# Kernel optimization log

Hardware: AMD Instinct MI355X
Metric: run time of the kernel (lower is better)

Reference implementation:

```python
import jax, jax.numpy as jnp
import numpy as np

B, D, H = 32768, 688, 4
DH = D // H          # 172 head dim (d_model // h, overrides ctor d_k)
MH = 128             # mlp hidden
EPS = 1e-5
SCALE = 1.0 / float(np.sqrt(DH))


def _ln(x, g, b):
    m = jnp.mean(x, -1, keepdims=True)
    v = jnp.var(x, -1, keepdims=True)  # biased var, matches torch LayerNorm
    return (x - m) / jnp.sqrt(v + EPS) * g + b


def setup_inputs() -> dict:
    key = jax.random.key(0)
    ks = jax.random.split(key, 16)
    w = lambda k, o, i: jax.random.normal(k, (o, i), jnp.float32) * 0.001  # init.normal_(std=0.001)
    z = lambda n: jnp.zeros((n,), jnp.float32)
    o = lambda n: jnp.ones((n,), jnp.float32)
    return dict(
        x=jax.random.normal(ks[0], (B, D), jnp.float32),
        x2=jax.random.normal(ks[1], (B, D), jnp.float32),
        Wq_v=w(ks[2], D, D), bq_v=z(D),
        Wk_v=w(ks[3], D, D), bk_v=z(D),
        Wv_v=w(ks[4], D, D), bv_v=z(D),
        Wq_i=w(ks[5], D, D), bq_i=z(D),
        Wk_i=w(ks[6], D, D), bk_i=z(D),
        Wv_i=w(ks[7], D, D), bv_i=z(D),
        Wo_v=w(ks[8], D, D), bo_v=z(D),
        Wo_i=w(ks[9], D, D), bo_i=z(D),
        ln1_g=o(D), ln1_b=z(D), ln2_g=o(D), ln2_b=z(D),
        ln3_g=o(D), ln3_b=z(D), ln4_g=o(D), ln4_b=z(D),
        m1v_W=w(ks[10], MH, D), m1v_b=z(MH),
        m2v_W=w(ks[11], D, MH), m2v_b=z(D),
        m1i_W=w(ks[12], MH, D), m1i_b=z(MH),
        m2i_W=w(ks[13], D, MH), m2i_b=z(D),
        coef=o(8),  # LearnableCoefficient 1..8, all init to 1.0
    )


def reference(x, x2,
              Wq_v, bq_v, Wk_v, bk_v, Wv_v, bv_v,
              Wq_i, bq_i, Wk_i, bk_i, Wv_i, bv_i,
              Wo_v, bo_v, Wo_i, bo_i,
              ln1_g, ln1_b, ln2_g, ln2_b, ln3_g, ln3_b, ln4_g, ln4_b,
              m1v_W, m1v_b, m2v_W, m2v_b, m1i_W, m1i_b, m2i_W, m2i_b,
              coef):
    rgb = _ln(x, ln1_g, ln1_b)
    ir = _ln(x2, ln2_g, ln2_b)
    proj = lambda t, W, b: (t @ W.T + b).reshape(-1, H, DH)  # (B, h, d_k)
    q_vis, k_vis, v_vis = proj(rgb, Wq_v, bq_v), proj(rgb, Wk_v, bk_v), proj(rgb, Wv_v, bv_v)
    q_ir, k_ir, v_ir = proj(ir, Wq_i, bq_i), proj(ir, Wk_i, bk_i), proj(ir, Wv_i, bv_i)
    # cross attention over heads: scores are (B, h, h)
    att_vis = jax.nn.softmax(jnp.einsum('bhd,bgd->bhg', q_ir, k_vis) * SCALE, -1)
    att_ir = jax.nn.softmax(jnp.einsum('bhd,bgd->bhg', q_vis, k_ir) * SCALE, -1)
    out_vis = jnp.einsum('bhg,bgd->bhd', att_vis, v_vis).reshape(-1, D) @ Wo_v.T + bo_v
    out_ir = jnp.einsum('bhg,bgd->bhd', att_ir, v_ir).reshape(-1, D) @ Wo_i.T + bo_i
    out_vis = coef[0] * x + coef[1] * out_vis
    out_ir = coef[2] * x2 + coef[3] * out_ir
    mv = jax.nn.gelu(_ln(out_vis, ln3_g, ln3_b) @ m1v_W.T + m1v_b, approximate=False) @ m2v_W.T + m2v_b
    mi = jax.nn.gelu(_ln(out_ir, ln4_g, ln4_b) @ m1i_W.T + m1i_b, approximate=False) @ m2i_W.T + m2i_b
    out_vis = coef[4] * out_vis + coef[5] * mv
    out_ir = coef[6] * out_ir + coef[7] * mi
    return out_vis, out_ir
```

## Files before the change

kernel.cpp:

```cpp
#include <hip/hip_runtime.h>
#include <cmath>


#define B_ROWS 32768
#define D_DIM  688
#define DP     704
#define DH_DIM 172
#define MH_DIM 128

typedef unsigned short ushort_t;
typedef __attribute__((ext_vector_type(8))) __bf16 bf16x8;
typedef __attribute__((ext_vector_type(4))) float  f32x4;

__device__ __forceinline__ float b2f(ushort_t u) {
    return __builtin_bit_cast(float, (unsigned int)u << 16);
}
__device__ __forceinline__ ushort_t f2bf(float f) {
    unsigned int u = __builtin_bit_cast(unsigned int, f);
    u += 0x7FFFu + ((u >> 16) & 1u);
    return (ushort_t)(u >> 16);
}

__device__ __forceinline__ void gl2lds16(const ushort_t* g, ushort_t* l) {
    __builtin_amdgcn_global_load_lds(
        (const __attribute__((address_space(1))) unsigned int*)g,
        (__attribute__((address_space(3))) unsigned int*)l, 16, 0, 0);
}

struct CvtJobs {
    const float* src[12];
    ushort_t*    dst[12];
    int O[12], Opad[12], Kin[12], Kpad[12];
    int bstart[13];
};

__global__ __launch_bounds__(256)
void cvt_all(CvtJobs jobs)
{
    int b = blockIdx.x;
    int j = 0;
    while (b >= jobs.bstart[j + 1]) ++j;
    const int t = (b - jobs.bstart[j]) * 256 + threadIdx.x;
    const int Kpad = jobs.Kpad[j];
    const int Kin  = jobs.Kin[j];
    const int cpr  = Kpad >> 3;
    if (t >= jobs.Opad[j] * cpr) return;
    const int o = t / cpr;
    const int c = t - o * cpr;
    unsigned int p0 = 0, p1 = 0, p2 = 0, p3 = 0;
    if (o < jobs.O[j] && (c * 8 + 8) <= Kin) {
        const float* s = jobs.src[j] + (size_t)o * Kin + c * 8;
        float4 f0 = reinterpret_cast<const float4*>(s)[0];
        float4 f1 = reinterpret_cast<const float4*>(s)[1];
        p0 = f2bf(f0.x) | ((unsigned int)f2bf(f0.y) << 16);
        p1 = f2bf(f0.z) | ((unsigned int)f2bf(f0.w) << 16);
        p2 = f2bf(f1.x) | ((unsigned int)f2bf(f1.y) << 16);
        p3 = f2bf(f1.z) | ((unsigned int)f2bf(f1.w) << 16);
    }
    *reinterpret_cast<uint4*>(jobs.dst[j] + (size_t)o * Kpad + c * 8) =
        make_uint4(p0, p1, p2, p3);
}

__global__ __launch_bounds__(256)
void pack_bias(const float* __restrict__ a0, const float* __restrict__ a1,
               const float* __restrict__ a2, const float* __restrict__ b0,
               const float* __restrict__ b1, const float* __restrict__ b2,
               float* __restrict__ dv, float* __restrict__ di)
{
    int t = blockIdx.x * 256 + threadIdx.x;
    if (t >= 2064) return;
    float v, w;
    if (t < 688)       { v = a0[t];        w = b0[t]; }
    else if (t < 1376) { v = a1[t - 688];  w = b1[t - 688]; }
    else               { v = a2[t - 1376]; w = b2[t - 1376]; }
    dv[t] = v; di[t] = w;
}

__global__ __launch_bounds__(256)
void ln_kernel(const float* __restrict__ Xv, const float* __restrict__ Xi,
               const float* __restrict__ gv, const float* __restrict__ bv,
               const float* __restrict__ gi, const float* __restrict__ bi,
               ushort_t* __restrict__ Yv, ushort_t* __restrict__ Yi)
{
    const int lane = threadIdx.x & 63;
    const int wave = threadIdx.x >> 6;
    const long w = (long)blockIdx.x * 4 + wave;
    const float* X; const float* g; const float* b; ushort_t* Y; long r;
    if (w < B_ROWS) { X = Xv; g = gv; b = bv; Y = Yv; r = w; }
    else            { X = Xi; g = gi; b = bi; Y = Yi; r = w - B_ROWS; }

    const float4* row = reinterpret_cast<const float4*>(X + r * D_DIM);
    float4 v0 = row[lane];
    float4 v1 = row[lane + 64];
    float4 v2 = make_float4(0.f, 0.f, 0.f, 0.f);
    if (lane < 44) v2 = row[lane + 128];

    float s  = v0.x + v0.y + v0.z + v0.w + v1.x + v1.y + v1.z + v1.w
             + v2.x + v2.y + v2.z + v2.w;
    float s2 = v0.x*v0.x + v0.y*v0.y + v0.z*v0.z + v0.w*v0.w
             + v1.x*v1.x + v1.y*v1.y + v1.z*v1.z + v1.w*v1.w
             + v2.x*v2.x + v2.y*v2.y + v2.z*v2.z + v2.w*v2.w;
#pragma unroll
    for (int m = 32; m; m >>= 1) { s += __shfl_xor(s, m); s2 += __shfl_xor(s2, m); }

    const float mean = s * (1.f / 688.f);
    const float var  = s2 * (1.f / 688.f) - mean * mean;
    const float rstd = rsqrtf(var + 1e-5f);

    const float4* g4 = reinterpret_cast<const float4*>(g);
    const float4* b4 = reinterpret_cast<const float4*>(b);
    ushort4* out4 = reinterpret_cast<ushort4*>(Y + r * DP);

    {
        float4 gg = g4[lane], bb = b4[lane];
        ushort4 o;
        o.x = f2bf((v0.x - mean) * rstd * gg.x + bb.x);
        o.y = f2bf((v0.y - mean) * rstd * gg.y + bb.y);
        o.z = f2bf((v0.z - mean) * rstd * gg.z + bb.z);
        o.w = f2bf((v0.w - mean) * rstd * gg.w + bb.w);
        out4[lane] = o;
    }
    {
        float4 gg = g4[lane + 64], bb = b4[lane + 64];
        ushort4 o;
        o.x = f2bf((v1.x - mean) * rstd * gg.x + bb.x);
        o.y = f2bf((v1.y - mean) * rstd * gg.y + bb.y);
        o.z = f2bf((v1.z - mean) * rstd * gg.z + bb.z);
        o.w = f2bf((v1.w - mean) * rstd * gg.w + bb.w);
        out4[lane + 64] = o;
    }
    if (lane < 44) {
        float4 gg = g4[lane + 128], bb = b4[lane + 128];
        ushort4 o;
        o.x = f2bf((v2.x - mean) * rstd * gg.x + bb.x);
        o.y = f2bf((v2.y - mean) * rstd * gg.y + bb.y);
        o.z = f2bf((v2.z - mean) * rstd * gg.z + bb.z);
        o.w = f2bf((v2.w - mean) * rstd * gg.w + bb.w);
        out4[lane + 128] = o;
    } else if (lane < 48) {
        out4[lane + 128] = make_ushort4(0, 0, 0, 0);
    }
}

template<int MODE>
__global__ __launch_bounds__(512, 2)
void gemmT(const ushort_t* __restrict__ A0, const ushort_t* __restrict__ A1,
           const ushort_t* __restrict__ W0, const ushort_t* __restrict__ W1,
           const float* __restrict__ bias0, const float* __restrict__ bias1,
           ushort_t* __restrict__ out0, ushort_t* __restrict__ out1,
           const float* __restrict__ res0, const float* __restrict__ res1,
           const float* __restrict__ coef, int ca0, int cb0, int ca1, int cb1,
           int NBn, int N, int K, int lda, int ldw, int ldo)
{
    __shared__ __align__(16) ushort_t lds[36864];

    const int q8 = gridDim.x >> 3;
    const int v  = (blockIdx.x & 7) * q8 + (blockIdx.x >> 3);
    const int nb = v % NBn;
    const int tmp = v / NBn;
    const int mb = tmp & 127;
    const int zz = tmp >> 7;

    const ushort_t* A = zz ? A1 : A0;
    const ushort_t* W = zz ? W1 : W0;
    const float* bias = zz ? bias1 : bias0;
    ushort_t* outp    = zz ? out1 : out0;
    const float* resid = zz ? res1 : res0;
    const int ca = zz ? ca1 : ca0;
    const int cb = zz ? cb1 : cb0;

    const int tid  = threadIdx.x;
    const int lane = tid & 63;
    const int wave = tid >> 6;
    const int wrow = wave >> 1;
    const int wcol = wave & 1;
    const int m0 = mb * 256;
    const int n0 = nb * 128;
    const int rl16 = lane & 15;
    const int q4   = lane >> 4;

    const int r0a  = tid >> 2;
    const int swzk = ((tid & 3) ^ ((tid >> 3) & 3)) * 8;

    f32x4 acc[4][4];
#pragma unroll
    for (int i = 0; i < 4; ++i)
#pragma unroll
        for (int j = 0; j < 4; ++j)
            acc[i][j] = f32x4{0.f, 0.f, 0.f, 0.f};

    const int NT = K >> 5;

#define STAGET(kt, bb) do {                                                        \
    const ushort_t* _sa = A + (size_t)(m0 + r0a) * lda + (kt)*32 + swzk;           \
    gl2lds16(_sa,                    lds + (bb)*12288 + wave*512);                 \
    gl2lds16(_sa + 128*(size_t)lda,  lds + (bb)*12288 + 4096 + wave*512);          \
    const ushort_t* _sb = W + (size_t)(n0 + r0a) * ldw + (kt)*32 + swzk;           \
    gl2lds16(_sb,                    lds + (bb)*12288 + 8192 + wave*512);          \
} while (0)

    STAGET(0, 0);
    STAGET(1, 1);
    asm volatile("s_waitcnt vmcnt(3)" ::: "memory");
    __builtin_amdgcn_s_barrier();

    for (int t = 0; t < NT; ++t) {
        const int cbuf = t % 3;
        const int pbuf = (t + 2) % 3;
        const int tn2 = (t + 2 < NT) ? t + 2 : NT - 1;

        bf16x8 af[4], bw[4];
#pragma unroll
        for (int i = 0; i < 4; ++i) {
            const int row_ = wrow * 64 + i * 16 + rl16;
            af[i] = *reinterpret_cast<const bf16x8*>(
                lds + cbuf * 12288 + row_ * 32 + ((q4 ^ ((row_ >> 1) & 3)) * 8));
        }
#pragma unroll
        for (int j = 0; j < 4; ++j) {
            const int row_ = wcol * 64 + j * 16 + rl16;
            bw[j] = *reinterpret_cast<const bf16x8*>(
                lds + cbuf * 12288 + 8192 + row_ * 32 + ((q4 ^ ((row_ >> 1) & 3)) * 8));
        }
        STAGET(tn2, pbuf);
        asm volatile("s_waitcnt vmcnt(3)" ::: "memory");
        __builtin_amdgcn_s_barrier();
        __builtin_amdgcn_s_setprio(1);
#pragma unroll
        for (int i = 0; i < 4; ++i)
#pragma unroll
            for (int j = 0; j < 4; ++j)
                acc[i][j] = __builtin_amdgcn_mfma_f32_16x16x32_bf16(af[i], bw[j], acc[i][j], 0, 0, 0);
        __builtin_amdgcn_s_setprio(0);
        __builtin_amdgcn_s_barrier();
    }

    asm volatile("s_waitcnt vmcnt(0)" ::: "memory");
    __builtin_amdgcn_s_barrier();

    ushort_t* const Cl = lds;
#pragma unroll
    for (int mi = 0; mi < 4; ++mi)
#pragma unroll
        for (int nj = 0; nj < 4; ++nj)
#pragma unroll
            for (int r = 0; r < 4; ++r) {
                const int row  = wrow * 64 + mi * 16 + q4 * 4 + r;
                const int colL = wcol * 64 + nj * 16 + rl16;
                const int blk  = (colL >> 3) ^ (((row >> 2) & 3) << 1);
                Cl[row * 128 + blk * 8 + (colL & 7)] = f2bf(acc[mi][nj][r]);
            }
    __syncthreads();

    float cA = 0.f, cB = 1.f;
    if constexpr (MODE == 1) { cA = coef[ca]; cB = coef[cb]; }
#pragma unroll
    for (int it2 = 0; it2 < 8; ++it2) {
        const int c   = it2 * 512 + tid;
        const int row = c >> 4;
        const int lb  = c & 15;
        const int gcol = n0 + lb * 8;
        if (gcol >= N) continue;
        const int pb = lb ^ (((row >> 2) & 3) << 1);
        uint4 pv = *reinterpret_cast<const uint4*>(Cl + row * 128 + pb * 8);
        const ushort_t* pu = (const ushort_t*)&pv;
        float4 b0 = *reinterpret_cast<const float4*>(bias + gcol);
        float4 b1 = *reinterpret_cast<const float4*>(bias + gcol + 4);
        const float bb[8] = {b0.x, b0.y, b0.z, b0.w, b1.x, b1.y, b1.z, b1.w};
        const size_t idx = (size_t)(m0 + row) * ldo + gcol;
        ushort_t o[8];
        if constexpr (MODE == 0) {
#pragma unroll
            for (int k = 0; k < 8; ++k) o[k] = f2bf(b2f(pu[k]) + bb[k]);
        } else {
            const float* rp = resid + idx;
            float4 r0_ = reinterpret_cast<const float4*>(rp)[0];
            float4 r1_ = reinterpret_cast<const float4*>(rp)[1];
            const float rr[8] = {r0_.x, r0_.y, r0_.z, r0_.w, r1_.x, r1_.y, r1_.z, r1_.w};
#pragma unroll
            for (int k = 0; k < 8; ++k)
                o[k] = f2bf(cA * rr[k] + cB * (b2f(pu[k]) + bb[k]));
        }
        *reinterpret_cast<uint4*>(outp + idx) = *reinterpret_cast<uint4*>(o);
    }
#undef STAGET
}

__global__ __launch_bounds__(256)
void mlp_fused(const ushort_t* __restrict__ ov0, const ushort_t* __restrict__ ov1,
               const float* __restrict__ g0, const float* __restrict__ b0,
               const float* __restrict__ g1, const float* __restrict__ b1,
               const ushort_t* __restrict__ W10, const ushort_t* __restrict__ W11,
               const float* __restrict__ mb10, const float* __restrict__ mb11,
               const ushort_t* __restrict__ W20, const ushort_t* __restrict__ W21,
               const float* __restrict__ mb20, const float* __restrict__ mb21,
               const float* __restrict__ coef,
               float* __restrict__ out0, float* __restrict__ out1)
{
    __shared__ __align__(16) ushort_t hraw[32 * 712];
    __shared__ __align__(16) ushort_t gbuf[32 * 136];
    __shared__ float glds[704];
    __shared__ float blds[704];
    __shared__ float mlds[32];
    __shared__ float rlds[32];

    const int zz = blockIdx.y;
    const ushort_t* ovb = zz ? ov1 : ov0;
    const float* lg = zz ? g1 : g0;
    const float* lb = zz ? b1 : b0;
    const ushort_t* W1 = zz ? W11 : W10;
    const float* mb1 = zz ? mb11 : mb10;
    const ushort_t* W2 = zz ? W21 : W20;
    const float* mb2 = zz ? mb21 : mb20;
    float* outp = zz ? out1 : out0;
    const float cA = coef[zz ? 6 : 4];
    const float cB = coef[zz ? 7 : 5];

    const int tid  = threadIdx.x;
    const int lane = tid & 63;
    const int wv   = tid >> 6;
    const long r0  = (long)blockIdx.x * 32;

    if (tid < 176) {
        float4 gg = make_float4(0, 0, 0, 0), bb = make_float4(0, 0, 0, 0);
        if (tid < 172) {
            gg = reinterpret_cast<const float4*>(lg)[tid];
            bb = reinterpret_cast<const float4*>(lb)[tid];
        }
        reinterpret_cast<float4*>(glds)[tid] = gg;
        reinterpret_cast<float4*>(blds)[tid] = bb;
    }

#pragma unroll
    for (int it = 0; it < 11; ++it) {
        const int c = it * 256 + tid;
        const int row = c / 88;
        const int u = c - row * 88;
        uint4 vv = make_uint4(0, 0, 0, 0);
        if (u < 86)
            vv = *reinterpret_cast<const uint4*>(ovb + (r0 + row) * 688 + u * 8);
        *reinterpret_cast<uint4*>(&hraw[row * 712 + u * 8]) = vv;
    }
    __syncthreads();

    for (int rr = 0; rr < 8; ++rr) {
        const int row = wv * 8 + rr;
        const ushort_t* hp = &hraw[row * 712];
        ushort4 a0 = *reinterpret_cast<const ushort4*>(hp + lane * 4);
        ushort4 a1 = *reinterpret_cast<const ushort4*>(hp + 256 + lane * 4);
        ushort4 a2 = make_ushort4(0, 0, 0, 0);
        if (lane < 44) a2 = *reinterpret_cast<const ushort4*>(hp + 512 + lane * 4);
        float e[12] = {b2f(a0.x), b2f(a0.y), b2f(a0.z), b2f(a0.w),
                       b2f(a1.x), b2f(a1.y), b2f(a1.z), b2f(a1.w),
                       b2f(a2.x), b2f(a2.y), b2f(a2.z), b2f(a2.w)};
        float s = 0.f, s2 = 0.f;
#pragma unroll
        for (int k = 0; k < 12; ++k) { s += e[k]; s2 += e[k] * e[k]; }
#pragma unroll
        for (int m = 32; m; m >>= 1) { s += __shfl_xor(s, m); s2 += __shfl_xor(s2, m); }
        if (lane == 0) {
            const float mean = s * (1.f / 688.f);
            const float var  = s2 * (1.f / 688.f) - mean * mean;
            mlds[row] = mean;
            rlds[row] = rsqrtf(var + 1e-5f);
        }
    }
    __syncthreads();

#pragma unroll
    for (int it = 0; it < 11; ++it) {
        const int c = it * 256 + tid;
        if (c < 2752) {
            const int row = c / 86;
            const int u = c - row * 86;
            uint4 vv = *reinterpret_cast<const uint4*>(&hraw[row * 712 + u * 8]);
            const float mean = mlds[row], rstd = rlds[row];
            const ushort_t* pe = (const ushort_t*)&vv;
            ushort_t o[8];
#pragma unroll
            for (int k = 0; k < 8; ++k)
                o[k] = f2bf((b2f(pe[k]) - mean) * rstd * glds[u * 8 + k] + blds[u * 8 + k]);
            *reinterpret_cast<uint4*>(&hraw[row * 712 + u * 8]) = *reinterpret_cast<uint4*>(o);
        }
    }
    __syncthreads();

    const int rl16 = lane & 15;
    const int q4   = lane >> 4;

    {
        f32x4 acc[2][2];
#pragma unroll
        for (int i = 0; i < 2; ++i) { acc[i][0] = f32x4{0,0,0,0}; acc[i][1] = f32x4{0,0,0,0}; }
        for (int kt = 0; kt < 11; ++kt) {
#pragma unroll
            for (int kk = 0; kk < 64; kk += 32) {
                bf16x8 af[2], bw[2];
#pragma unroll
                for (int n = 0; n < 2; ++n)
                    bw[n] = *reinterpret_cast<const bf16x8*>(
                        W1 + (size_t)(wv * 32 + n * 16 + rl16) * 704 + kt * 64 + kk + q4 * 8);
#pragma unroll
                for (int i = 0; i < 2; ++i)
                    af[i] = *reinterpret_cast<const bf16x8*>(
                        &hraw[(i * 16 + rl16) * 712 + kt * 64 + kk + q4 * 8]);
#pragma unroll
                for (int i = 0; i < 2; ++i)
#pragma unroll
                    for (int n = 0; n < 2; ++n)
                        acc[i][n] = __builtin_amdgcn_mfma_f32_16x16x32_bf16(
                            af[i], bw[n], acc[i][n], 0, 0, 0);
            }
        }
        const int rb = q4 * 4;
#pragma unroll
        for (int n = 0; n < 2; ++n) {
            const int col = wv * 32 + n * 16 + rl16;
            const float bc = mb1[col];
#pragma unroll
            for (int i = 0; i < 2; ++i)
#pragma unroll
                for (int r = 0; r < 4; ++r) {
                    float val = acc[i][n][r] + bc;
                    val = 0.5f * val * (1.0f + erff(val * 0.70710678118654752f));
                    gbuf[(i * 16 + rb + r) * 136 + col] = f2bf(val);
                }
        }
    }
    __syncthreads();

    for (int ch = 0; ch < 11; ++ch) {
        const int col16 = wv * 176 + ch * 16;
        if (col16 >= 688) continue;
        f32x4 acc2[2];
        acc2[0] = f32x4{0, 0, 0, 0};
        acc2[1] = f32x4{0, 0, 0, 0};
#pragma unroll
        for (int kk = 0; kk < 4; ++kk) {
            bf16x8 bw2 = *reinterpret_cast<const bf16x8*>(
                W2 + (size_t)(col16 + rl16) * 128 + kk * 32 + q4 * 8);
            bf16x8 af2[2];
#pragma unroll
            for (int i = 0; i < 2; ++i)
                af2[i] = *reinterpret_cast<const bf16x8*>(
                    &gbuf[(i * 16 + rl16) * 136 + kk * 32 + q4 * 8]);
#pragma unroll
            for (int i = 0; i < 2; ++i)
                acc2[i] = __builtin_amdgcn_mfma_f32_16x16x32_bf16(af2[i], bw2, acc2[i], 0, 0, 0);
        }
        const int col = col16 + rl16;
        const float bc = mb2[col];
#pragma unroll
        for (int i = 0; i < 2; ++i)
#pragma unroll
            for (int r = 0; r < 4; ++r) {
                const long row = r0 + i * 16 + q4 * 4 + r;
                const float raw = b2f(ovb[row * 688 + col]);
                outp[row * 688 + col] = cA * raw + cB * (acc2[i][r] + bc);
            }
    }
}

__global__ __launch_bounds__(256)
void attn_kernel(const ushort_t* __restrict__ qkv_v, const ushort_t* __restrict__ qkv_i,
                 ushort_t* __restrict__ ctx_v, ushort_t* __restrict__ ctx_i)
{
    const int lane = threadIdx.x & 63;
    const int wave = threadIdx.x >> 6;
    const long r = (long)blockIdx.x * 4 + wave;
    const ushort_t* bv = qkv_v + r * 2064;
    const ushort_t* bi = qkv_i + r * 2064;

    float sv[4][4], si[4][4];
#pragma unroll
    for (int h = 0; h < 4; ++h)
#pragma unroll
        for (int g = 0; g < 4; ++g) { sv[h][g] = 0.f; si[h][g] = 0.f; }

    float vvr[3][4], vir[3][4];
#pragma unroll
    for (int it = 0; it < 3; ++it) {
        const int d = lane + it * 64;
        const bool ok = d < DH_DIM;
        float qv[4], kv[4], qi[4], ki[4];
#pragma unroll
        for (int h = 0; h < 4; ++h) {
            const int o = h * DH_DIM + d;
            qv[h]      = ok ? b2f(bv[o]) : 0.f;
            kv[h]      = ok ? b2f(bv[D_DIM + o]) : 0.f;
            vvr[it][h] = ok ? b2f(bv[2 * D_DIM + o]) : 0.f;
            qi[h]      = ok ? b2f(bi[o]) : 0.f;
            ki[h]      = ok ? b2f(bi[D_DIM + o]) : 0.f;
            vir[it][h] = ok ? b2f(bi[2 * D_DIM + o]) : 0.f;
        }
#pragma unroll
        for (int h = 0; h < 4; ++h)
#pragma unroll
            for (int g = 0; g < 4; ++g) {
                sv[h][g] += qi[h] * kv[g];
                si[h][g] += qv[h] * ki[g];
            }
    }

#pragma unroll
    for (int h = 0; h < 4; ++h)
#pragma unroll
        for (int g = 0; g < 4; ++g) {
            float a = sv[h][g], b = si[h][g];
#pragma unroll
            for (int m = 32; m; m >>= 1) { a += __shfl_xor(a, m); b += __shfl_xor(b, m); }
            sv[h][g] = a; si[h][g] = b;
        }

    const float scale = 0.07624928516630235f;
    float av[4][4], ai[4][4];
#pragma unroll
    for (int h = 0; h < 4; ++h) {
        float m1 = fmaxf(fmaxf(sv[h][0], sv[h][1]), fmaxf(sv[h][2], sv[h][3])) * scale;
        float m2 = fmaxf(fmaxf(si[h][0], si[h][1]), fmaxf(si[h][2], si[h][3])) * scale;
        float d1 = 0.f, d2 = 0.f;
#pragma unroll
        for (int g = 0; g < 4; ++g) {
            av[h][g] = expf(sv[h][g] * scale - m1); d1 += av[h][g];
            ai[h][g] = expf(si[h][g] * scale - m2); d2 += ai[h][g];
        }
        const float r1 = 1.f / d1, r2 = 1.f / d2;
#pragma unroll
        for (int g = 0; g < 4; ++g) { av[h][g] *= r1; ai[h][g] *= r2; }
    }

#pragma unroll
    for (int it = 0; it < 3; ++it) {
        const int d = lane + it * 64;
        if (d < DH_DIM) {
#pragma unroll
            for (int h = 0; h < 4; ++h) {
                float cv = av[h][0] * vvr[it][0] + av[h][1] * vvr[it][1]
                         + av[h][2] * vvr[it][2] + av[h][3] * vvr[it][3];
                float ci = ai[h][0] * vir[it][0] + ai[h][1] * vir[it][1]
                         + ai[h][2] * vir[it][2] + ai[h][3] * vir[it][3];
                ctx_v[r * DP + h * DH_DIM + d] = f2bf(cv);
                ctx_i[r * DP + h * DH_DIM + d] = f2bf(ci);
            }
        }
    }
    if (lane < 16) {
        ctx_v[r * DP + 688 + lane] = 0;
        ctx_i[r * DP + 688 + lane] = 0;
    }
}

extern "C" void kernel_launch(void* const* d_in, const int* in_sizes, int n_in,
                              void* d_out, int out_size, void* d_ws, size_t ws_size,
                              hipStream_t stream)
{
    if (n_in < 35) return;
    const float* x     = (const float*)d_in[0];
    const float* x2    = (const float*)d_in[1];
    const float* Wq_v  = (const float*)d_in[2];
    const float* bq_v  = (const float*)d_in[3];
    const float* Wk_v  = (const float*)d_in[4];
    const float* bk_v  = (const float*)d_in[5];
    const float* Wv_v  = (const float*)d_in[6];
    const float* bv_v  = (const float*)d_in[7];
    const float* Wq_i  = (const float*)d_in[8];
    const float* bq_i  = (const float*)d_in[9];
    const float* Wk_i  = (const float*)d_in[10];
    const float* bk_i  = (const float*)d_in[11];
    const float* Wv_i  = (const float*)d_in[12];
    const float* bv_i  = (const float*)d_in[13];
    const float* Wo_v  = (const float*)d_in[14];
    const float* bo_v  = (const float*)d_in[15];
    const float* Wo_i  = (const float*)d_in[16];
    const float* bo_i  = (const float*)d_in[17];
    const float* ln1_g = (const float*)d_in[18];
    const float* ln1_b = (const float*)d_in[19];
    const float* ln2_g = (const float*)d_in[20];
    const float* ln2_b = (const float*)d_in[21];
    const float* ln3_g = (const float*)d_in[22];
    const float* ln3_b = (const float*)d_in[23];
    const float* ln4_g = (const float*)d_in[24];
    const float* ln4_b = (const float*)d_in[25];
    const float* m1v_W = (const float*)d_in[26];
    const float* m1v_b = (const float*)d_in[27];
    const float* m2v_W = (const float*)d_in[28];
    const float* m2v_b = (const float*)d_in[29];
    const float* m1i_W = (const float*)d_in[30];
    const float* m1i_b = (const float*)d_in[31];
    const float* m2i_W = (const float*)d_in[32];
    const float* m2i_b = (const float*)d_in[33];
    const float* coef  = (const float*)d_in[34];

    const size_t BDP = (size_t)B_ROWS * DP;
    const size_t BD  = (size_t)B_ROWS * D_DIM;

    char* ws = (char*)d_ws;
    size_t off = 0;
    auto give = [&](size_t bytes) {
        char* p = ws + off;
        off += (bytes + 255) & ~(size_t)255;
        return p;
    };
    ushort_t* Wcat_v = (ushort_t*)give(2304ull * DP * 2);
    ushort_t* Wcat_i = (ushort_t*)give(2304ull * DP * 2);
    ushort_t* Wo_vb  = (ushort_t*)give(768ull * DP * 2);
    ushort_t* Wo_ib  = (ushort_t*)give(768ull * DP * 2);
    ushort_t* m1vb   = (ushort_t*)give(128ull * DP * 2);
    ushort_t* m1ib   = (ushort_t*)give(128ull * DP * 2);
    ushort_t* m2vb   = (ushort_t*)give(768ull * 128 * 2);
    ushort_t* m2ib   = (ushort_t*)give(768ull * 128 * 2);
    float*    bcat_v = (float*)give(2064 * 4);
    float*    bcat_i = (float*)give(2064 * 4);
    char* regX = give(BDP * 2 * 2);
    char* regQ = give((size_t)B_ROWS * 2064 * 2 * 2);
    if (ws_size < off) return;

    ushort_t* xn_v  = (ushort_t*)regX;
    ushort_t* xn_i  = xn_v + BDP;
    ushort_t* ctx_v = xn_v;
    ushort_t* ctx_i = xn_i;
    ushort_t* qkv_v = (ushort_t*)regQ;
    ushort_t* qkv_i = qkv_v + (size_t)B_ROWS * 2064;
    ushort_t* ovb   = (ushort_t*)regQ;
    ushort_t* oib   = ovb + BD;

    float* ov = (float*)d_out;
    float* oi = ov + BD;

    CvtJobs J;
    const float* srcs[12] = {Wq_v, Wk_v, Wv_v, Wq_i, Wk_i, Wv_i,
                             Wo_v, Wo_i, m1v_W, m1i_W, m2v_W, m2i_W};
    ushort_t* dsts[12] = {Wcat_v, Wcat_v + 688 * DP, Wcat_v + 1376 * DP,
                          Wcat_i, Wcat_i + 688 * DP, Wcat_i + 1376 * DP,
                          Wo_vb, Wo_ib, m1vb, m1ib, m2vb, m2ib};
    int Os[12]    = {688, 688, 688, 688, 688, 688, 688, 688, 128, 128, 688, 688};
    int Opads[12] = {688, 688, 800, 688, 688, 800, 768, 768, 128, 128, 768, 768};
    int Kins[12]  = {688, 688, 688, 688, 688, 688, 688, 688, 688, 688, 128, 128};
    int Kpads[12] = {DP, DP, DP, DP, DP, DP, DP, DP, DP, DP, 128, 128};
    int bs = 0;
    for (int j = 0; j < 12; ++j) {
        J.src[j] = srcs[j]; J.dst[j] = dsts[j];
        J.O[j] = Os[j]; J.Opad[j] = Opads[j]; J.Kin[j] = Kins[j]; J.Kpad[j] = Kpads[j];
        J.bstart[j] = bs;
        bs += (Opads[j] * (Kpads[j] >> 3) + 255) / 256;
    }
    J.bstart[12] = bs;
    cvt_all<<<dim3(bs), dim3(256), 0, stream>>>(J);

    pack_bias<<<dim3(9), dim3(256), 0, stream>>>(bq_v, bk_v, bv_v, bq_i, bk_i, bv_i,
                                                 bcat_v, bcat_i);

    ln_kernel<<<dim3(2 * B_ROWS / 4), dim3(256), 0, stream>>>(
        x, x2, ln1_g, ln1_b, ln2_g, ln2_b, xn_v, xn_i);

    gemmT<0><<<dim3(128 * 17 * 2), dim3(512), 0, stream>>>(
        xn_v, xn_i, Wcat_v, Wcat_i, bcat_v, bcat_i, qkv_v, qkv_i,
        nullptr, nullptr, nullptr, 0, 0, 0, 0, 17, 2064, DP, DP, DP, 2064);

    attn_kernel<<<dim3(B_ROWS / 4), dim3(256), 0, stream>>>(qkv_v, qkv_i, ctx_v, ctx_i);

    gemmT<1><<<dim3(128 * 6 * 2), dim3(512), 0, stream>>>(
        ctx_v, ctx_i, Wo_vb, Wo_ib, bo_v, bo_i, ovb, oib,
        x, x2, coef, 0, 1, 2, 3, 6, 688, DP, DP, DP, 688);

    mlp_fused<<<dim3(B_ROWS / 32, 2), dim3(256), 0, stream>>>(
        ovb, oib, ln3_g, ln3_b, ln4_g, ln4_b,
        m1vb, m1ib, m1v_b, m1i_b, m2vb, m2ib, m2v_b, m2i_b,
        coef, ov, oi);
}
```

Measured before the change: 689.7 us.

## Halve GEMM block to 4 waves with larger per-wave tiles; stage attention rows via LDS

The GEMM now runs 256 threads per block for the same 256x128 tile. Each wave computes a 128x64 sub-tile with 8x4 MFMA accumulators and issues twice as many async global-to-LDS loads per stage, with the wait counts adjusted to match. This aims for more MFMA work per LDS fragment load and fewer waves contending for barriers, at the cost of higher register pressure. Separately, the attention kernel bulk-copies its four rows of qkv into LDS and has each lane read 4-wide vectors of 4 consecutive head-dim elements, replacing scalar strided global loads and stores with vectorized ones.

Result: slower. 717.4 us (+4.0%).

```diff
diff --git a/kernel.cpp b/kernel.cpp
--- a/kernel.cpp
+++ b/kernel.cpp
@@ -143,7 +143,7 @@
 }
 
 template<int MODE>
-__global__ __launch_bounds__(512, 2)
+__global__ __launch_bounds__(256, 2)
 void gemmT(const ushort_t* __restrict__ A0, const ushort_t* __restrict__ A1,
            const ushort_t* __restrict__ W0, const ushort_t* __restrict__ W1,
            const float* __restrict__ bias0, const float* __restrict__ bias1,
@@ -179,12 +179,12 @@
     const int rl16 = lane & 15;
     const int q4   = lane >> 4;
 
-    const int r0a  = tid >> 2;
-    const int swzk = ((tid & 3) ^ ((tid >> 3) & 3)) * 8;
-
-    f32x4 acc[4][4];
-#pragma unroll
-    for (int i = 0; i < 4; ++i)
+    const int r0a  = (wave * 64 + lane) >> 2;
+    const int swzk = ((lane & 3) ^ ((lane >> 3) & 3)) * 8;
+
+    f32x4 acc[8][4];
+#pragma unroll
+    for (int i = 0; i < 8; ++i)
 #pragma unroll
         for (int j = 0; j < 4; ++j)
             acc[i][j] = f32x4{0.f, 0.f, 0.f, 0.f};
@@ -192,16 +192,19 @@
     const int NT = K >> 5;
 
 #define STAGET(kt, bb) do {                                                        \
-    const ushort_t* _sa = A + (size_t)(m0 + r0a) * lda + (kt)*32 + swzk;           \
-    gl2lds16(_sa,                    lds + (bb)*12288 + wave*512);                 \
-    gl2lds16(_sa + 128*(size_t)lda,  lds + (bb)*12288 + 4096 + wave*512);          \
-    const ushort_t* _sb = W + (size_t)(n0 + r0a) * ldw + (kt)*32 + swzk;           \
-    gl2lds16(_sb,                    lds + (bb)*12288 + 8192 + wave*512);          \
+    const ushort_t* _a = A + (size_t)(m0 + r0a) * lda + (kt)*32 + swzk;            \
+    gl2lds16(_a,                     lds + (bb)*12288 + wave*512);                 \
+    gl2lds16(_a +  64*(size_t)lda,   lds + (bb)*12288 + 2048 + wave*512);          \
+    gl2lds16(_a + 128*(size_t)lda,   lds + (bb)*12288 + 4096 + wave*512);          \
+    gl2lds16(_a + 192*(size_t)lda,   lds + (bb)*12288 + 6144 + wave*512);          \
+    const ushort_t* _b = W + (size_t)(n0 + r0a) * ldw + (kt)*32 + swzk;            \
+    gl2lds16(_b,                     lds + (bb)*12288 + 8192 + wave*512);          \
+    gl2lds16(_b +  64*(size_t)ldw,   lds + (bb)*12288 + 10240 + wave*512);         \
 } while (0)
 
     STAGET(0, 0);
     STAGET(1, 1);
-    asm volatile("s_waitcnt vmcnt(3)" ::: "memory");
+    asm volatile("s_waitcnt vmcnt(6)" ::: "memory");
     __builtin_amdgcn_s_barrier();
 
     for (int t = 0; t < NT; ++t) {
@@ -209,10 +212,10 @@
         const int pbuf = (t + 2) % 3;
         const int tn2 = (t + 2 < NT) ? t + 2 : NT - 1;
 
-        bf16x8 af[4], bw[4];
-#pragma unroll
-        for (int i = 0; i < 4; ++i) {
-            const int row_ = wrow * 64 + i * 16 + rl16;
+        bf16x8 af[8], bw[4];
+#pragma unroll
+        for (int i = 0; i < 8; ++i) {
+            const int row_ = wrow * 128 + i * 16 + rl16;
             af[i] = *reinterpret_cast<const bf16x8*>(
                 lds + cbuf * 12288 + row_ * 32 + ((q4 ^ ((row_ >> 1) & 3)) * 8));
         }
@@ -223,11 +226,11 @@
                 lds + cbuf * 12288 + 8192 + row_ * 32 + ((q4 ^ ((row_ >> 1) & 3)) * 8));
         }
         STAGET(tn2, pbuf);
-        asm volatile("s_waitcnt vmcnt(3)" ::: "memory");
+        asm volatile("s_waitcnt vmcnt(6)" ::: "memory");
         __builtin_amdgcn_s_barrier();
         __builtin_amdgcn_s_setprio(1);
 #pragma unroll
-        for (int i = 0; i < 4; ++i)
+        for (int i = 0; i < 8; ++i)
 #pragma unroll
             for (int j = 0; j < 4; ++j)
                 acc[i][j] = __builtin_amdgcn_mfma_f32_16x16x32_bf16(af[i], bw[j], acc[i][j], 0, 0, 0);
@@ -240,12 +243,12 @@
 
     ushort_t* const Cl = lds;
 #pragma unroll
-    for (int mi = 0; mi < 4; ++mi)
+    for (int mi = 0; mi < 8; ++mi)
 #pragma unroll
         for (int nj = 0; nj < 4; ++nj)
 #pragma unroll
             for (int r = 0; r < 4; ++r) {
-                const int row  = wrow * 64 + mi * 16 + q4 * 4 + r;
+                const int row  = wrow * 128 + mi * 16 + q4 * 4 + r;
                 const int colL = wcol * 64 + nj * 16 + rl16;
                 const int blk  = (colL >> 3) ^ (((row >> 2) & 3) << 1);
                 Cl[row * 128 + blk * 8 + (colL & 7)] = f2bf(acc[mi][nj][r]);
@@ -255,8 +258,8 @@
     float cA = 0.f, cB = 1.f;
     if constexpr (MODE == 1) { cA = coef[ca]; cB = coef[cb]; }
 #pragma unroll
-    for (int it2 = 0; it2 < 8; ++it2) {
-        const int c   = it2 * 512 + tid;
+    for (int it2 = 0; it2 < 16; ++it2) {
+        const int c   = it2 * 256 + tid;
         const int row = c >> 4;
         const int lb  = c & 15;
         const int gcol = n0 + lb * 8;
@@ -465,48 +468,61 @@
 void attn_kernel(const ushort_t* __restrict__ qkv_v, const ushort_t* __restrict__ qkv_i,
                  ushort_t* __restrict__ ctx_v, ushort_t* __restrict__ ctx_i)
 {
-    const int lane = threadIdx.x & 63;
-    const int wave = threadIdx.x >> 6;
-    const long r = (long)blockIdx.x * 4 + wave;
-    const ushort_t* bv = qkv_v + r * 2064;
-    const ushort_t* bi = qkv_i + r * 2064;
+    __shared__ __align__(16) ushort_t sm[16896];
+
+    const int tid  = threadIdx.x;
+    const int lane = tid & 63;
+    const int wv   = tid >> 6;
+    const long r0  = (long)blockIdx.x * 4;
+
+#pragma unroll
+    for (int i = 0; i < 9; ++i) {
+        int c = i * 256 + wv * 64 + lane;
+        if (c > 2063) c = 2063;
+        const int row = c / 516;
+        const int s = c - row * 516;
+        const ushort_t* src = (s < 258)
+            ? qkv_v + (r0 + row) * 2064 + s * 8
+            : qkv_i + (r0 + row) * 2064 + (s - 258) * 8;
+        gl2lds16(src, sm + (size_t)(i * 256 + wv * 64) * 8);
+    }
+    __syncthreads();
+
+    const ushort_t* bv = sm + wv * 4128;
+    const ushort_t* bi = bv + 2064;
+    const bool act = lane < 43;
+    const int d4 = lane * 4;
+
+    float qv[4][4], kv[4][4], vv[4][4], qi[4][4], ki[4][4], vi[4][4];
+#pragma unroll
+    for (int h = 0; h < 4; ++h) {
+        const int o = h * DH_DIM + d4;
+        ushort4 z = make_ushort4(0, 0, 0, 0);
+        ushort4 a = act ? *reinterpret_cast<const ushort4*>(bv + o)        : z;
+        ushort4 b = act ? *reinterpret_cast<const ushort4*>(bv + 688 + o)  : z;
+        ushort4 c = act ? *reinterpret_cast<const ushort4*>(bv + 1376 + o) : z;
+        ushort4 d = act ? *reinterpret_cast<const ushort4*>(bi + o)        : z;
+        ushort4 e = act ? *reinterpret_cast<const ushort4*>(bi + 688 + o)  : z;
+        ushort4 f = act ? *reinterpret_cast<const ushort4*>(bi + 1376 + o) : z;
+        qv[h][0]=b2f(a.x); qv[h][1]=b2f(a.y); qv[h][2]=b2f(a.z); qv[h][3]=b2f(a.w);
+        kv[h][0]=b2f(b.x); kv[h][1]=b2f(b.y); kv[h][2]=b2f(b.z); kv[h][3]=b2f(b.w);
+        vv[h][0]=b2f(c.x); vv[h][1]=b2f(c.y); vv[h][2]=b2f(c.z); vv[h][3]=b2f(c.w);
+        qi[h][0]=b2f(d.x); qi[h][1]=b2f(d.y); qi[h][2]=b2f(d.z); qi[h][3]=b2f(d.w);
+        ki[h][0]=b2f(e.x); ki[h][1]=b2f(e.y); ki[h][2]=b2f(e.z); ki[h][3]=b2f(e.w);
+        vi[h][0]=b2f(f.x); vi[h][1]=b2f(f.y); vi[h][2]=b2f(f.z); vi[h][3]=b2f(f.w);
+    }
 
     float sv[4][4], si[4][4];
 #pragma unroll
     for (int h = 0; h < 4; ++h)
 #pragma unroll
-        for (int g = 0; g < 4; ++g) { sv[h][g] = 0.f; si[h][g] = 0.f; }
-
-    float vvr[3][4], vir[3][4];
-#pragma unroll
-    for (int it = 0; it < 3; ++it) {
-        const int d = lane + it * 64;
-        const bool ok = d < DH_DIM;
-        float qv[4], kv[4], qi[4], ki[4];
-#pragma unroll
-        for (int h = 0; h < 4; ++h) {
-            const int o = h * DH_DIM + d;
-            qv[h]      = ok ? b2f(bv[o]) : 0.f;
-            kv[h]      = ok ? b2f(bv[D_DIM + o]) : 0.f;
-            vvr[it][h] = ok ? b2f(bv[2 * D_DIM + o]) : 0.f;
-            qi[h]      = ok ? b2f(bi[o]) : 0.f;
-            ki[h]      = ok ? b2f(bi[D_DIM + o]) : 0.f;
-            vir[it][h] = ok ? b2f(bi[2 * D_DIM + o]) : 0.f;
-        }
-#pragma unroll
-        for (int h = 0; h < 4; ++h)
-#pragma unroll
-            for (int g = 0; g < 4; ++g) {
-                sv[h][g] += qi[h] * kv[g];
-                si[h][g] += qv[h] * ki[g];
+        for (int g = 0; g < 4; ++g) {
+            float a = 0.f, b = 0.f;
+#pragma unroll
+            for (int e = 0; e < 4; ++e) {
+                a += qi[h][e] * kv[g][e];
+                b += qv[h][e] * ki[g][e];
             }
-    }
-
-#pragma unroll
-    for (int h = 0; h < 4; ++h)
-#pragma unroll
-        for (int g = 0; g < 4; ++g) {
-            float a = sv[h][g], b = si[h][g];
 #pragma unroll
             for (int m = 32; m; m >>= 1) { a += __shfl_xor(a, m); b += __shfl_xor(b, m); }
             sv[h][g] = a; si[h][g] = b;
@@ -529,24 +545,27 @@
         for (int g = 0; g < 4; ++g) { av[h][g] *= r1; ai[h][g] *= r2; }
     }
 
-#pragma unroll
-    for (int it = 0; it < 3; ++it) {
-        const int d = lane + it * 64;
-        if (d < DH_DIM) {
-#pragma unroll
-            for (int h = 0; h < 4; ++h) {
-                float cv = av[h][0] * vvr[it][0] + av[h][1] * vvr[it][1]
-                         + av[h][2] * vvr[it][2] + av[h][3] * vvr[it][3];
-                float ci = ai[h][0] * vir[it][0] + ai[h][1] * vir[it][1]
-                         + ai[h][2] * vir[it][2] + ai[h][3] * vir[it][3];
-                ctx_v[r * DP + h * DH_DIM + d] = f2bf(cv);
-                ctx_i[r * DP + h * DH_DIM + d] = f2bf(ci);
+    const long r = r0 + wv;
+#pragma unroll
+    for (int h = 0; h < 4; ++h) {
+        if (act) {
+            ushort4 ov_, oi_;
+            float c0, c1;
+#pragma unroll
+            for (int e = 0; e < 4; ++e) {
+                c0 = av[h][0]*vv[0][e] + av[h][1]*vv[1][e] + av[h][2]*vv[2][e] + av[h][3]*vv[3][e];
+                c1 = ai[h][0]*vi[0][e] + ai[h][1]*vi[1][e] + ai[h][2]*vi[2][e] + ai[h][3]*vi[3][e];
+                ((ushort_t*)&ov_)[e] = f2bf(c0);
+                ((ushort_t*)&oi_)[e] = f2bf(c1);
             }
-        }
-    }
-    if (lane < 16) {
-        ctx_v[r * DP + 688 + lane] = 0;
-        ctx_i[r * DP + 688 + lane] = 0;
+            *reinterpret_cast<ushort4*>(ctx_v + r * DP + h * DH_DIM + d4) = ov_;
+            *reinterpret_cast<ushort4*>(ctx_i + r * DP + h * DH_DIM + d4) = oi_;
+        }
+    }
+    if (lane >= 44 && lane < 48) {
+        const int o = 688 + (lane - 44) * 4;
+        *reinterpret_cast<ushort4*>(ctx_v + r * DP + o) = make_ushort4(0, 0, 0, 0);
+        *reinterpret_cast<ushort4*>(ctx_i + r * DP + o) = make_ushort4(0, 0, 0, 0);
     }
 }
 
@@ -653,13 +672,13 @@
     ln_kernel<<<dim3(2 * B_ROWS / 4), dim3(256), 0, stream>>>(
         x, x2, ln1_g, ln1_b, ln2_g, ln2_b, xn_v, xn_i);
 
-    gemmT<0><<<dim3(128 * 17 * 2), dim3(512), 0, stream>>>(
+    gemmT<0><<<dim3(128 * 17 * 2), dim3(256), 0, stream>>>(
         xn_v, xn_i, Wcat_v, Wcat_i, bcat_v, bcat_i, qkv_v, qkv_i,
         nullptr, nullptr, nullptr, 0, 0, 0, 0, 17, 2064, DP, DP, DP, 2064);
 
     attn_kernel<<<dim3(B_ROWS / 4), dim3(256), 0, stream>>>(qkv_v, qkv_i, ctx_v, ctx_i);
 
-    gemmT<1><<<dim3(128 * 6 * 2), dim3(512), 0, stream>>>(
+    gemmT<1><<<dim3(128 * 6 * 2), dim3(256), 0, stream>>>(
         ctx_v, ctx_i, Wo_vb, Wo_ib, bo_v, bo_i, ovb, oib,
         x, x2, coef, 0, 1, 2, 3, 6, 688, DP, DP, DP, 688);
 
```

## Halve GEMM block to 4 waves with 128x64 warp tiles and prefetched fragments

Applied to the files above, without the earlier changes.

The bf16 GEMM kernel now uses 256 threads (4 waves) per block, and each wave computes a 128x64 output tile (8x4 MFMA accumulators) instead of 64x64. Global-to-LDS staging is spread over six loads per thread. LDS fragment reads for the next k-step are issued after the current MFMAs, which removes the trailing barrier per iteration. The aim is higher MFMA-to-LDS-read reuse and less barrier overhead per step. In exchange, accumulator register pressure doubles, which may cut occupancy or cause spills.

Result: no change. 685.3 us (-0.6%).

```diff
diff --git a/kernel.cpp b/kernel.cpp
--- a/kernel.cpp
+++ b/kernel.cpp
@@ -143,7 +143,7 @@
 }
 
 template<int MODE>
-__global__ __launch_bounds__(512, 2)
+__global__ __launch_bounds__(256, 2)
 void gemmT(const ushort_t* __restrict__ A0, const ushort_t* __restrict__ A1,
            const ushort_t* __restrict__ W0, const ushort_t* __restrict__ W1,
            const float* __restrict__ bias0, const float* __restrict__ bias1,
@@ -179,12 +179,12 @@
     const int rl16 = lane & 15;
     const int q4   = lane >> 4;
 
-    const int r0a  = tid >> 2;
-    const int swzk = ((tid & 3) ^ ((tid >> 3) & 3)) * 8;
-
-    f32x4 acc[4][4];
-#pragma unroll
-    for (int i = 0; i < 4; ++i)
+    const int r0a  = (wave * 64 + lane) >> 2;
+    const int swzk = ((lane & 3) ^ ((lane >> 3) & 3)) * 8;
+
+    f32x4 acc[8][4];
+#pragma unroll
+    for (int i = 0; i < 8; ++i)
 #pragma unroll
         for (int j = 0; j < 4; ++j)
             acc[i][j] = f32x4{0.f, 0.f, 0.f, 0.f};
@@ -192,60 +192,64 @@
     const int NT = K >> 5;
 
 #define STAGET(kt, bb) do {                                                        \
-    const ushort_t* _sa = A + (size_t)(m0 + r0a) * lda + (kt)*32 + swzk;           \
-    gl2lds16(_sa,                    lds + (bb)*12288 + wave*512);                 \
-    gl2lds16(_sa + 128*(size_t)lda,  lds + (bb)*12288 + 4096 + wave*512);          \
-    const ushort_t* _sb = W + (size_t)(n0 + r0a) * ldw + (kt)*32 + swzk;           \
-    gl2lds16(_sb,                    lds + (bb)*12288 + 8192 + wave*512);          \
+    const ushort_t* _a = A + (size_t)(m0 + r0a) * lda + (kt)*32 + swzk;            \
+    gl2lds16(_a,                     lds + (bb)*12288 + wave*512);                 \
+    gl2lds16(_a +  64*(size_t)lda,   lds + (bb)*12288 + 2048 + wave*512);          \
+    gl2lds16(_a + 128*(size_t)lda,   lds + (bb)*12288 + 4096 + wave*512);          \
+    gl2lds16(_a + 192*(size_t)lda,   lds + (bb)*12288 + 6144 + wave*512);          \
+    const ushort_t* _b = W + (size_t)(n0 + r0a) * ldw + (kt)*32 + swzk;            \
+    gl2lds16(_b,                     lds + (bb)*12288 + 8192 + wave*512);          \
+    gl2lds16(_b +  64*(size_t)ldw,   lds + (bb)*12288 + 10240 + wave*512);         \
 } while (0)
+
+#define RDFRAG(bb) do {                                                            \
+    _Pragma("unroll")                                                              \
+    for (int i = 0; i < 8; ++i) {                                                  \
+        const int row_ = wrow * 128 + i * 16 + rl16;                               \
+        af[i] = *reinterpret_cast<const bf16x8*>(                                  \
+            lds + (bb) * 12288 + row_ * 32 + ((q4 ^ ((row_ >> 1) & 3)) * 8));      \
+    }                                                                              \
+    _Pragma("unroll")                                                              \
+    for (int j = 0; j < 4; ++j) {                                                  \
+        const int row_ = wcol * 64 + j * 16 + rl16;                                \
+        bw[j] = *reinterpret_cast<const bf16x8*>(                                  \
+            lds + (bb) * 12288 + 8192 + row_ * 32 + ((q4 ^ ((row_ >> 1) & 3)) * 8)); \
+    } } while (0)
+
+    bf16x8 af[8], bw[4];
 
     STAGET(0, 0);
     STAGET(1, 1);
-    asm volatile("s_waitcnt vmcnt(3)" ::: "memory");
+    asm volatile("s_waitcnt vmcnt(6)" ::: "memory");
     __builtin_amdgcn_s_barrier();
+    RDFRAG(0);
 
     for (int t = 0; t < NT; ++t) {
-        const int cbuf = t % 3;
-        const int pbuf = (t + 2) % 3;
         const int tn2 = (t + 2 < NT) ? t + 2 : NT - 1;
-
-        bf16x8 af[4], bw[4];
-#pragma unroll
-        for (int i = 0; i < 4; ++i) {
-            const int row_ = wrow * 64 + i * 16 + rl16;
-            af[i] = *reinterpret_cast<const bf16x8*>(
-                lds + cbuf * 12288 + row_ * 32 + ((q4 ^ ((row_ >> 1) & 3)) * 8));
-        }
-#pragma unroll
-        for (int j = 0; j < 4; ++j) {
-            const int row_ = wcol * 64 + j * 16 + rl16;
-            bw[j] = *reinterpret_cast<const bf16x8*>(
-                lds + cbuf * 12288 + 8192 + row_ * 32 + ((q4 ^ ((row_ >> 1) & 3)) * 8));
-        }
-        STAGET(tn2, pbuf);
-        asm volatile("s_waitcnt vmcnt(3)" ::: "memory");
+        STAGET(tn2, (t + 2) % 3);
+        asm volatile("s_waitcnt vmcnt(6)" ::: "memory");
+        asm volatile("s_waitcnt lgkmcnt(0)" ::: "memory");
         __builtin_amdgcn_s_barrier();
         __builtin_amdgcn_s_setprio(1);
 #pragma unroll
-        for (int i = 0; i < 4; ++i)
+        for (int i = 0; i < 8; ++i)
 #pragma unroll
             for (int j = 0; j < 4; ++j)
                 acc[i][j] = __builtin_amdgcn_mfma_f32_16x16x32_bf16(af[i], bw[j], acc[i][j], 0, 0, 0);
         __builtin_amdgcn_s_setprio(0);
-        __builtin_amdgcn_s_barrier();
-    }
-
-    asm volatile("s_waitcnt vmcnt(0)" ::: "memory");
-    __builtin_amdgcn_s_barrier();
+        if (t + 1 < NT) RDFRAG((t + 1) % 3);
+    }
+
+    __syncthreads();
 
     ushort_t* const Cl = lds;
 #pragma unroll
-    for (int mi = 0; mi < 4; ++mi)
+    for (int mi = 0; mi < 8; ++mi)
 #pragma unroll
         for (int nj = 0; nj < 4; ++nj)
 #pragma unroll
             for (int r = 0; r < 4; ++r) {
-                const int row  = wrow * 64 + mi * 16 + q4 * 4 + r;
+                const int row  = wrow * 128 + mi * 16 + q4 * 4 + r;
                 const int colL = wcol * 64 + nj * 16 + rl16;
                 const int blk  = (colL >> 3) ^ (((row >> 2) & 3) << 1);
                 Cl[row * 128 + blk * 8 + (colL & 7)] = f2bf(acc[mi][nj][r]);
@@ -255,8 +259,8 @@
     float cA = 0.f, cB = 1.f;
     if constexpr (MODE == 1) { cA = coef[ca]; cB = coef[cb]; }
 #pragma unroll
-    for (int it2 = 0; it2 < 8; ++it2) {
-        const int c   = it2 * 512 + tid;
+    for (int it2 = 0; it2 < 16; ++it2) {
+        const int c   = it2 * 256 + tid;
         const int row = c >> 4;
         const int lb  = c & 15;
         const int gcol = n0 + lb * 8;
@@ -284,6 +288,7 @@
         *reinterpret_cast<uint4*>(outp + idx) = *reinterpret_cast<uint4*>(o);
     }
 #undef STAGET
+#undef RDFRAG
 }
 
 __global__ __launch_bounds__(256)
@@ -653,13 +658,13 @@
     ln_kernel<<<dim3(2 * B_ROWS / 4), dim3(256), 0, stream>>>(
         x, x2, ln1_g, ln1_b, ln2_g, ln2_b, xn_v, xn_i);
 
-    gemmT<0><<<dim3(128 * 17 * 2), dim3(512), 0, stream>>>(
+    gemmT<0><<<dim3(128 * 17 * 2), dim3(256), 0, stream>>>(
         xn_v, xn_i, Wcat_v, Wcat_i, bcat_v, bcat_i, qkv_v, qkv_i,
         nullptr, nullptr, nullptr, 0, 0, 0, 0, 17, 2064, DP, DP, DP, 2064);
 
     attn_kernel<<<dim3(B_ROWS / 4), dim3(256), 0, stream>>>(qkv_v, qkv_i, ctx_v, ctx_i);
 
-    gemmT<1><<<dim3(128 * 6 * 2), dim3(512), 0, stream>>>(
+    gemmT<1><<<dim3(128 * 6 * 2), dim3(256), 0, stream>>>(
         ctx_v, ctx_i, Wo_vb, Wo_ib, bo_v, bo_i, ovb, oib,
         x, x2, coef, 0, 1, 2, 3, 6, 688, DP, DP, DP, 688);
 
```
